# Kernel optimization log

Measured on AMD Instinct MI355X. Metric: run time of the kernel, lower is better.

Reference implementation:

```python
import jax, jax.numpy as jnp
import numpy as np

N = 30000      # node_size / new_node_size
R = 1000       # rel_size
T = 300000     # triple_size (edges)
D = 128        # node_hid == rel_hid
B = 1024       # train pairs
NNZ = 600000   # nnz of ent_adj / rel_adj
DEPTH = 2
GAMMA = 3.0
EPS = 1e-12    # F.normalize eps


def setup_inputs():
    key = jax.random.key(0)
    ks = jax.random.split(key, 12)
    adj = jnp.stack([jax.random.randint(ks[0], (T,), 0, N),
                     jax.random.randint(ks[1], (T,), 0, N)]).astype(jnp.int64)
    # one relation per triple: row ids are 0..T-1, col ids are relation ids
    r_index = jnp.stack([jnp.arange(T),
                         jax.random.randint(ks[2], (T,), 0, R)]).astype(jnp.int64)
    r_val = jnp.ones((T,), jnp.float32)
    ent_adj = jnp.stack([jax.random.randint(ks[3], (NNZ,), 0, N),
                         jax.random.randint(ks[4], (NNZ,), 0, N)]).astype(jnp.int64)
    rel_adj = jnp.stack([jax.random.randint(ks[5], (NNZ,), 0, N),
                         jax.random.randint(ks[6], (NNZ,), 0, R)]).astype(jnp.int64)
    ent_emb = jax.random.normal(ks[7], (N, D), jnp.float32) * 0.05
    rel_emb = jax.random.normal(ks[8], (R, D), jnp.float32) * 0.05
    attn_e = jax.random.normal(ks[9], (DEPTH, D, 1), jnp.float32) * 0.1
    attn_r = jax.random.normal(ks[10], (DEPTH, D, 1), jnp.float32) * 0.1
    train_pairs = jax.random.randint(ks[11], (B, 2), 0, N).astype(jnp.int64)
    return dict(ent_emb=ent_emb, rel_emb=rel_emb, attn_e=attn_e, attn_r=attn_r,
                r_val=r_val, adj=adj, r_index=r_index, ent_adj=ent_adj,
                rel_adj=rel_adj, train_pairs=train_pairs)


def _segment_softmax(vals, seg, num):
    m = jax.ops.segment_max(vals, seg, num_segments=num)
    e = jnp.exp(vals - m[seg])
    s = jax.ops.segment_sum(e, seg, num_segments=num)
    return e / s[seg]


def _avg(adj, emb):
    # sparse softmax of an all-ones matrix over dim=1 == 1/deg per nonzero, then spmm
    row, col = adj[0], adj[1]
    deg = jax.ops.segment_sum(jnp.ones_like(row, emb.dtype), row, num_segments=N)
    return jax.ops.segment_sum(emb[col] / deg[row][:, None], row, num_segments=N)


def _gat(features, rel_emb, adj, r_index, r_val, kernels):
    features = jnp.tanh(features)
    outputs = [features]
    row, col = adj[0], adj[1]
    for l in range(DEPTH):
        # sparse [T,R] @ rel_emb  -> per-triple relation embedding
        tri_rel = jax.ops.segment_sum(r_val[:, None] * rel_emb[r_index[1]],
                                      r_index[0], num_segments=T)          # [T,D]
        tri_rel = tri_rel / jnp.maximum(
            jnp.linalg.norm(tri_rel, axis=1, keepdims=True), EPS)
        neighs = features[col]                                             # [T,D]
        neighs = neighs - 2.0 * jnp.sum(neighs * tri_rel, axis=1,
                                        keepdims=True) * tri_rel
        att = jnp.squeeze(tri_rel @ kernels[l], axis=-1)                   # [T]
        att = _segment_softmax(att, row, N)
        new_features = jax.ops.segment_sum(neighs * att[:, None], row,
                                           num_segments=N)
        features = jnp.tanh(new_features)
        outputs.append(features)
    return jnp.concatenate(outputs, axis=-1)  # [N, (DEPTH+1)*D]


def _align_loss(pairs, emb):
    l, r = pairs[:, 0], pairs[:, 1]
    l_emb, r_emb = emb[l], emb[r]
    pos = jnp.sum(jnp.square(l_emb - r_emb), axis=-1, keepdims=True)       # [B,1]

    def sqdist(A, Bm):
        return (jnp.sum(jnp.square(A), axis=1)[:, None]
                + jnp.sum(jnp.square(Bm), axis=1)[None, :]
                - 2.0 * A @ Bm.T)

    bi = jnp.arange(pairs.shape[0])
    mask = jnp.ones((pairs.shape[0], N), emb.dtype)
    mask = mask.at[bi, l].add(-1.0).at[bi, r].add(-1.0)  # 1 - onehot(l) - onehot(r)

    def norm_lse(loss):
        mu = jax.lax.stop_gradient(jnp.mean(loss, axis=-1, keepdims=True))
        sd = jax.lax.stop_gradient(jnp.std(loss, axis=-1, keepdims=True))
        loss = (loss - mu) / sd
        return jax.nn.logsumexp(20.0 * loss + 8.0, axis=-1)

    l_loss = norm_lse((pos - sqdist(l_emb, emb) + GAMMA) * mask)
    r_loss = norm_lse((pos - sqdist(r_emb, emb) + GAMMA) * mask)
    return jnp.mean(l_loss + r_loss)


def reference(ent_emb, rel_emb, attn_e, attn_r, r_val, adj, r_index,
              ent_adj, rel_adj, train_pairs):
    ent_feature = _avg(ent_adj, ent_emb)   # [N,D]
    rel_feature = _avg(rel_adj, rel_emb)   # [N,D]
    out_rel = _gat(rel_feature, rel_emb, adj, r_index, r_val, attn_r)
    out_ent = _gat(ent_feature, rel_emb, adj, r_index, r_val, attn_e)
    emb = jnp.concatenate([out_ent, out_rel], axis=-1)  # [N, 6*D]
    return _align_loss(train_pairs, emb)
```

## Files before the change

### kernel.cpp

```cpp
#include <hip/hip_runtime.h>
#include <math.h>

#define N_ENT 30000
#define R_REL 1000
#define T_EDGE 300000
#define B_PAIR 1024
#define NNZ_E 600000
#define GAMMAF 3.0f
#define EPSV 1e-12f
#define EMBD 768
#define NPAD 30720
#define NT128 240
#define PTILES 480

typedef _Float16 half8 __attribute__((ext_vector_type(8)));
typedef _Float16 half4v __attribute__((ext_vector_type(4)));
typedef _Float16 half2v __attribute__((ext_vector_type(2)));
typedef float f32x4 __attribute__((ext_vector_type(4)));

__device__ inline void gl_lds16(const _Float16* g, _Float16* l){
  __builtin_amdgcn_global_load_lds(
      (const __attribute__((address_space(1))) unsigned int*)g,
      (__attribute__((address_space(3))) unsigned int*)l, 16, 0, 0);
}

__device__ inline float waveRedSum(float v){
  #pragma unroll
  for(int m=32;m>=1;m>>=1) v += __shfl_xor(v, m, 64);
  return v;
}

__device__ inline float fast_tanh(float x){
  x = fminf(10.f, fmaxf(-10.f, x));
  float e = __expf(2.f*x);
  return (e-1.f)/(e+1.f);
}

__global__ __launch_bounds__(256) void k_count3(const int* __restrict__ rA, int* cA,
                                                const int* __restrict__ rE, int* cE,
                                                const int* __restrict__ rR, int* cR){
  int e = blockIdx.x*256 + threadIdx.x;
  if(e < T_EDGE) atomicAdd(&cA[rA[e]], 1);
  if(e < NNZ_E){ atomicAdd(&cE[rE[e]], 1); atomicAdd(&cR[rR[e]], 1); }
}

__global__ __launch_bounds__(1024) void k_scan3(const int* c0, int* s0, int* u0,
                                                const int* c1, int* s1, int* u1,
                                                const int* c2, int* s2, int* u2){
  const int* cnt = blockIdx.x==0 ? c0 : (blockIdx.x==1 ? c1 : c2);
  int* start     = blockIdx.x==0 ? s0 : (blockIdx.x==1 ? s1 : s2);
  int* cursor    = blockIdx.x==0 ? u0 : (blockIdx.x==1 ? u1 : u2);
  __shared__ int wsum[16];
  __shared__ int carry;
  int tid = threadIdx.x, lane = tid & 63, wid = tid >> 6;
  if(tid==0) carry = 0;
  __syncthreads();
  for(int base=0; base<N_ENT; base+=1024){
    int i = base + tid;
    int v = (i<N_ENT)? cnt[i] : 0;
    int x = v;
    #pragma unroll
    for(int off=1; off<64; off<<=1){ int t=__shfl_up(x,off,64); if(lane>=off) x+=t; }
    if(lane==63) wsum[wid]=x;
    __syncthreads();
    if(wid==0){
      int s = (lane<16)? wsum[lane] : 0;
      #pragma unroll
      for(int off=1; off<16; off<<=1){ int t=__shfl_up(s,off,64); if(lane>=off) s+=t; }
      if(lane<16) wsum[lane]=s;
    }
    __syncthreads();
    int wexcl = (wid==0)? 0 : wsum[wid-1];
    int excl = carry + wexcl + x - v;
    if(i<N_ENT){ start[i]=excl; cursor[i]=excl; }
    int tot = wsum[15];
    __syncthreads();
    if(tid==0) carry += tot;
    __syncthreads();
  }
  if(tid==0) start[N_ENT] = carry;
}

__global__ __launch_bounds__(256) void k_scatter3(
      const int* __restrict__ rA, const int* __restrict__ cAj, const int* __restrict__ rid,
      int* uA, int* scolA, int* sridA,
      const int* __restrict__ rE, const int* __restrict__ cEj, int* uE, int* scolE,
      const int* __restrict__ rR, const int* __restrict__ cRj, int* uR, int* scolR){
  int e = blockIdx.x*256 + threadIdx.x;
  if(e < T_EDGE){
    int p = atomicAdd(&uA[rA[e]], 1);
    scolA[p] = cAj[e];
    sridA[p] = rid[e];
  }
  if(e < NNZ_E){
    int p = atomicAdd(&uE[rE[e]], 1);
    scolE[p] = cEj[e];
    int q = atomicAdd(&uR[rR[e]], 1);
    scolR[q] = cRj[e];
  }
}

__global__ __launch_bounds__(256) void k_avg_tanh(const int* __restrict__ start, const int* __restrict__ scol,
                        const float* __restrict__ src, _Float16* featC, _Float16* Eh, int pairOff, int coloff){
  int r = blockIdx.x*4 + (threadIdx.x>>6);
  int lane = threadIdx.x & 63;
  int s0 = start[r], s1 = start[r+1];
  float ax=0.f, ay=0.f;
  int e = s0;
  for(; e+1<s1; e+=2){
    int c0 = scol[e], c1 = scol[e+1];
    float2 v0 = *(const float2*)(src + (size_t)c0*128 + lane*2);
    float2 v1 = *(const float2*)(src + (size_t)c1*128 + lane*2);
    ax += v0.x + v1.x; ay += v0.y + v1.y;
  }
  if(e<s1){
    int c0 = scol[e];
    float2 v0 = *(const float2*)(src + (size_t)c0*128 + lane*2);
    ax += v0.x; ay += v0.y;
  }
  float inv = (s1>s0) ? 1.0f/(float)(s1-s0) : 0.f;
  float vx = fast_tanh(ax*inv), vy = fast_tanh(ay*inv);
  half2v hv = {(_Float16)vx, (_Float16)vy};
  *(half2v*)(featC + (size_t)r*256 + lane*4 + pairOff) = hv;
  *(half2v*)(Eh + (size_t)r*EMBD + coloff + lane*2) = hv;
}

__global__ __launch_bounds__(256) void k_relnorm(const float* __restrict__ rel, const float* __restrict__ ae,
                          const float* __restrict__ ar, _Float16* relnH, float* expdot){
  int r = (blockIdx.x*256 + threadIdx.x) >> 6;
  int lane = threadIdx.x & 63;
  if (r >= R_REL) return;
  float2 v = *(const float2*)(rel + (size_t)r*128 + lane*2);
  float ss = waveRedSum(v.x*v.x + v.y*v.y);
  float nrm = fmaxf(sqrtf(ss), EPSV);
  float2 u; u.x = v.x/nrm; u.y = v.y/nrm;
  half2v uh = {(_Float16)u.x, (_Float16)u.y};
  *(half2v*)(relnH + (size_t)r*128 + lane*2) = uh;
  const float* ks[4] = {ae, ae+128, ar, ar+128};
  #pragma unroll
  for(int k=0;k<4;k++){
    float2 w = *(const float2*)(ks[k] + lane*2);
    float d = waveRedSum(u.x*w.x + u.y*w.y);
    if(lane==0) expdot[k*R_REL + r] = __expf(d);
  }
}

__global__ __launch_bounds__(256) void k_edge2(const int* __restrict__ start, const int* __restrict__ scol,
      const int* __restrict__ srid, const _Float16* __restrict__ relnH,
      const float* __restrict__ expE, const float* __restrict__ expR,
      const _Float16* __restrict__ featIn, _Float16* featOut, _Float16* Eh, int colEnt, int colRel){
  int r = blockIdx.x*4 + (threadIdx.x>>6);
  int lane = threadIdx.x & 63;
  int s0 = start[r], s1 = start[r+1];
  float aEx=0,aEy=0,aRx=0,aRy=0, swE=0, swR=0;
  int e = s0;
  for(; e+1<s1; e+=2){
    int c0=scol[e], q0=srid[e], c1=scol[e+1], q1=srid[e+1];
    float wE0=expE[q0], wR0=expR[q0], wE1=expE[q1], wR1=expR[q1];
    half2v u0h = *(const half2v*)(relnH + (size_t)q0*128 + lane*2);
    half2v u1h = *(const half2v*)(relnH + (size_t)q1*128 + lane*2);
    half4v h0 = *(const half4v*)(featIn + (size_t)c0*256 + lane*4);
    half4v h1 = *(const half4v*)(featIn + (size_t)c1*256 + lane*4);
    float u0x=(float)u0h[0], u0y=(float)u0h[1], u1x=(float)u1h[0], u1y=(float)u1h[1];
    float e0x=(float)h0[0], e0y=(float)h0[1], r0x=(float)h0[2], r0y=(float)h0[3];
    float e1x=(float)h1[0], e1y=(float)h1[1], r1x=(float)h1[2], r1y=(float)h1[3];
    float d0 = e0x*u0x + e0y*u0y;
    float d1 = r0x*u0x + r0y*u0y;
    float d2 = e1x*u1x + e1y*u1y;
    float d3 = r1x*u1x + r1y*u1y;
    #pragma unroll
    for(int m=32;m>=1;m>>=1){
      d0 += __shfl_xor(d0,m,64); d1 += __shfl_xor(d1,m,64);
      d2 += __shfl_xor(d2,m,64); d3 += __shfl_xor(d3,m,64);
    }
    aEx += wE0*(e0x - 2.f*d0*u0x) + wE1*(e1x - 2.f*d2*u1x);
    aEy += wE0*(e0y - 2.f*d0*u0y) + wE1*(e1y - 2.f*d2*u1y);
    aRx += wR0*(r0x - 2.f*d1*u0x) + wR1*(r1x - 2.f*d3*u1x);
    aRy += wR0*(r0y - 2.f*d1*u0y) + wR1*(r1y - 2.f*d3*u1y);
    swE += wE0+wE1; swR += wR0+wR1;
  }
  if(e<s1){
    int c0=scol[e], q0=srid[e];
    float wE0=expE[q0], wR0=expR[q0];
    half2v u0h = *(const half2v*)(relnH + (size_t)q0*128 + lane*2);
    half4v h0 = *(const half4v*)(featIn + (size_t)c0*256 + lane*4);
    float u0x=(float)u0h[0], u0y=(float)u0h[1];
    float e0x=(float)h0[0], e0y=(float)h0[1], r0x=(float)h0[2], r0y=(float)h0[3];
    float d0 = e0x*u0x + e0y*u0y;
    float d1 = r0x*u0x + r0y*u0y;
    #pragma unroll
    for(int m=32;m>=1;m>>=1){ d0 += __shfl_xor(d0,m,64); d1 += __shfl_xor(d1,m,64); }
    aEx += wE0*(e0x - 2.f*d0*u0x);
    aEy += wE0*(e0y - 2.f*d0*u0y);
    aRx += wR0*(r0x - 2.f*d1*u0x);
    aRy += wR0*(r0y - 2.f*d1*u0y);
    swE += wE0; swR += wR0;
  }
  float iE = (s1>s0) ? 1.f/swE : 0.f;
  float iR = (s1>s0) ? 1.f/swR : 0.f;
  float vEx = fast_tanh(aEx*iE), vEy = fast_tanh(aEy*iE);
  float vRx = fast_tanh(aRx*iR), vRy = fast_tanh(aRy*iR);
  half4v ov = {(_Float16)vEx,(_Float16)vEy,(_Float16)vRx,(_Float16)vRy};
  *(half4v*)(featOut + (size_t)r*256 + lane*4) = ov;
  half2v he = {(_Float16)vEx,(_Float16)vEy};
  half2v hr = {(_Float16)vRx,(_Float16)vRy};
  *(half2v*)(Eh + (size_t)r*EMBD + colEnt + lane*2) = he;
  *(half2v*)(Eh + (size_t)r*EMBD + colRel + lane*2) = hr;
}

__global__ __launch_bounds__(256) void k_gather(const _Float16* __restrict__ Eh, const int* __restrict__ tp,
                         _Float16* Wh, float* cvec){
  int i = blockIdx.x; int tid = threadIdx.x;
  int l = tp[2*i], r = tp[2*i+1];
  float sl=0.f, sr=0.f, sp=0.f;
  for(int c=tid;c<EMBD;c+=256){
    _Float16 lh = Eh[(size_t)l*EMBD+c], rh = Eh[(size_t)r*EMBD+c];
    float le = (float)lh, re = (float)rh;
    Wh[(size_t)i*EMBD+c]=lh; Wh[(size_t)(B_PAIR+i)*EMBD+c]=rh;
    sl += le*le; sr += re*re; float d = le-re; sp += d*d;
  }
  __shared__ float s0[256], s1[256], s2[256];
  s0[tid]=sl; s1[tid]=sr; s2[tid]=sp;
  __syncthreads();
  for(int w=128;w>0;w>>=1){
    if(tid<w){ s0[tid]+=s0[tid+w]; s1[tid]+=s1[tid+w]; s2[tid]+=s2[tid+w]; }
    __syncthreads();
  }
  if(tid==0){
    float pos = s2[0];
    cvec[i]        = pos + GAMMAF - s0[0];
    cvec[B_PAIR+i] = pos + GAMMAF - s1[0];
  }
}

__global__ __launch_bounds__(256) void k_qn(const _Float16* __restrict__ Eh, float* qn){
  int j = (blockIdx.x*256 + threadIdx.x) >> 6;
  int lane = threadIdx.x & 63;
  if(j >= NPAD) return;
  if(j >= N_ENT){ if(lane==0) qn[j] = 1e30f; return; }
  float s=0.f;
  #pragma unroll
  for(int q=0;q<12;q++){ float v = (float)Eh[(size_t)j*EMBD + lane + 64*q]; s += v*v; }
  s = waveRedSum(s);
  if(lane==0) qn[j]=s;
}

__global__ __launch_bounds__(256) void k_embstats(const _Float16* __restrict__ Eh, const float* __restrict__ qn,
                           float* Svec, float* Pvec, float* QQ){
  int tid = threadIdx.x;
  int n0 = blockIdx.x*32;
  int nend = n0+32; if(nend > N_ENT) nend = N_ENT;
  float s[3]={0,0,0}, p[3]={0,0,0};
  float q1=0.f, q2=0.f;
  for(int n=n0;n<nend;n++){
    float qv = qn[n];
    if(tid==0){ q1 += qv; q2 += qv*qv; }
    #pragma unroll
    for(int k=0;k<3;k++){
      float v = (float)Eh[(size_t)n*EMBD + tid + k*256];
      s[k] += v; p[k] += qv*v;
    }
  }
  #pragma unroll
  for(int k=0;k<3;k++){
    unsafeAtomicAdd(&Svec[tid + k*256], s[k]);
    unsafeAtomicAdd(&Pvec[tid + k*256], p[k]);
  }
  if(tid==0){ unsafeAtomicAdd(&QQ[0], q1); unsafeAtomicAdd(&QQ[1], q2); }
}

__global__ __launch_bounds__(256) void k_transp(const _Float16* __restrict__ Eh, _Float16* embT){
  __shared__ __align__(16) _Float16 til[64][72];
  int r0 = blockIdx.x*64, c0 = blockIdx.y*64;
  int t = threadIdx.x;
  int rr = t>>3, c8 = (t&7)*8;
  #pragma unroll
  for(int p=0;p<2;p++){
    int gr = r0 + rr + p*32;
    uint4 v = make_uint4(0u,0u,0u,0u);
    if(gr < N_ENT) v = *(const uint4*)(Eh + (size_t)gr*EMBD + c0 + c8);
    *(uint4*)&til[rr + p*32][c8] = v;
  }
  __syncthreads();
  #pragma unroll
  for(int p=0;p<2;p++){
    int cc = rr + p*32;
    __align__(16) _Float16 tmp[8];
    #pragma unroll
    for(int j=0;j<8;j++) tmp[j] = til[c8 + j][cc];
    *(uint4*)(embT + (size_t)(c0+cc)*NPAD + r0 + c8) = *(uint4*)tmp;
  }
}

__global__ __launch_bounds__(256) void k_syrk(const _Float16* __restrict__ embT, float* G){
  __shared__ __align__(16) _Float16 As[128*64];
  __shared__ __align__(16) _Float16 Bs[128*64];
  int tid = threadIdx.x;
  int w = tid>>6, lane = tid&63;
  int quad = lane>>4, l15 = lane&15;
  int lr = lane>>3, lc = lane&7;
  int wm = (w>>1)*64, wn = (w&1)*64;
  int m0 = blockIdx.y*128, n0 = blockIdx.x*128;
  int kbeg = blockIdx.z*3840;
  int kend = kbeg + 3840; if(kend > NPAD) kend = NPAD;
  f32x4 acc[4][4];
  #pragma unroll
  for(int i=0;i<4;i++)
    #pragma unroll
    for(int j=0;j<4;j++) acc[i][j] = (f32x4){0.f,0.f,0.f,0.f};
  for(int k0=kbeg;k0<kend;k0+=64){
    #pragma unroll
    for(int p=0;p<4;p++){
      int r = p*32 + w*8 + lr;
      int cg = lc ^ (r&7);
      gl_lds16(embT + (size_t)(m0+r)*NPAD + k0 + cg*8, As + (p*32 + w*8)*64);
      gl_lds16(embT + (size_t)(n0+r)*NPAD + k0 + cg*8, Bs + (p*32 + w*8)*64);
    }
    __syncthreads();
    #pragma unroll
    for(int ks=0;ks<2;ks++){
      half8 af[4], bf[4];
      #pragma unroll
      for(int i=0;i<4;i++){
        int ml = wm + i*16 + l15;
        af[i] = *(half8*)(As + ml*64 + (((ks<<2)|quad) ^ (ml&7))*8);
      }
      #pragma unroll
      for(int j=0;j<4;j++){
        int nl = wn + j*16 + l15;
        bf[j] = *(half8*)(Bs + nl*64 + (((ks<<2)|quad) ^ (nl&7))*8);
      }
      #pragma unroll
      for(int i=0;i<4;i++)
        #pragma unroll
        for(int j=0;j<4;j++)
          acc[i][j] = __builtin_amdgcn_mfma_f32_16x16x32_f16(af[i], bf[j], acc[i][j], 0,0,0);
    }
    __syncthreads();
  }
  #pragma unroll
  for(int i=0;i<4;i++){
    #pragma unroll
    for(int r=0;r<4;r++){
      int m = m0 + wm + i*16 + quad*4 + r;
      #pragma unroll
      for(int j=0;j<4;j++){
        int n = n0 + wn + j*16 + l15;
        unsafeAtomicAdd(&G[(size_t)m*EMBD + n], acc[i][j][r]);
      }
    }
  }
}

__global__ __launch_bounds__(256) void k_cvtG(const float* __restrict__ G, _Float16* Gh){
  int i = blockIdx.x*256 + threadIdx.x;
  if(i < EMBD*EMBD) Gh[i] = (_Float16)G[i];
}

__device__ inline void mfma_k768(const _Float16* __restrict__ Asrc, const _Float16* __restrict__ Bsrc,
                                 int m0, int n0, int l15, int quad, f32x4 acc[4][4]){
  const _Float16* aB[4]; const _Float16* bB[4];
  #pragma unroll
  for(int i=0;i<4;i++){
    aB[i] = Asrc + (size_t)(m0+i*16+l15)*EMBD + quad*8;
    bB[i] = Bsrc + (size_t)(n0+i*16+l15)*EMBD + quad*8;
  }
  half8 af[2][4], bf[2][4];
  #pragma unroll
  for(int i=0;i<4;i++){ af[0][i] = *(const half8*)(aB[i]); bf[0][i] = *(const half8*)(bB[i]); }
  #pragma unroll
  for(int ks=0; ks<24; ks++){
    int cur = ks&1, nxt = cur^1;
    if(ks<23){
      int ko = (ks+1)*32;
      #pragma unroll
      for(int i=0;i<4;i++){ af[nxt][i] = *(const half8*)(aB[i]+ko); bf[nxt][i] = *(const half8*)(bB[i]+ko); }
    }
    #pragma unroll
    for(int i=0;i<4;i++)
      #pragma unroll
      for(int j=0;j<4;j++)
        acc[i][j] = __builtin_amdgcn_mfma_f32_16x16x32_f16(af[cur][i], bf[cur][j], acc[i][j], 0,0,0);
  }
}

__global__ __launch_bounds__(256) void k_gemmTh(const _Float16* __restrict__ Wh, const _Float16* __restrict__ Gh,
                                                float* Tm){
  int tid = threadIdx.x, w = tid>>6, lane = tid&63;
  int quad = lane>>4, l15 = lane&15;
  int n0 = blockIdx.x*64;
  #pragma unroll
  for(int half=0; half<2; half++){
    int mt = blockIdx.y*8 + half*4 + w;
    int m0 = mt*64;
    f32x4 acc[4][4];
    #pragma unroll
    for(int i=0;i<4;i++)
      #pragma unroll
      for(int j=0;j<4;j++) acc[i][j] = (f32x4){0.f,0.f,0.f,0.f};
    mfma_k768(Wh, Gh, m0, n0, l15, quad, acc);
    #pragma unroll
    for(int i=0;i<4;i++)
      #pragma unroll
      for(int r=0;r<4;r++){
        int mg = m0 + i*16 + quad*4 + r;
        #pragma unroll
        for(int j=0;j<4;j++)
          Tm[(size_t)mg*EMBD + n0 + j*16 + l15] = acc[i][j][r];
      }
  }
}

__global__ __launch_bounds__(256) void k_rowstats(const _Float16* __restrict__ Wh, const float* __restrict__ Tm,
      const _Float16* __restrict__ Eh, const float* __restrict__ qn, const float* __restrict__ cvec,
      const int* __restrict__ tp, const float* __restrict__ Svec, const float* __restrict__ Pvec,
      const float* __restrict__ QQ, float* alpha, float* betav){
  int row = blockIdx.x*4 + (threadIdx.x>>6);
  int lane = threadIdx.x & 63;
  if(row >= 2*B_PAIR) return;
  int pi = row & (B_PAIR-1);
  int lp = tp[2*pi], rp = tp[2*pi+1];
  float d1=0,d2=0,d3=0,dl=0,dr=0;
  #pragma unroll
  for(int k=0;k<12;k++){
    int d = lane + 64*k;
    float a = (float)Wh[(size_t)row*EMBD + d];
    d1 += a*Svec[d];
    d2 += a*Pvec[d];
    d3 += a*Tm[(size_t)row*EMBD + d];
    dl += a*(float)Eh[(size_t)lp*EMBD + d];
    dr += a*(float)Eh[(size_t)rp*EMBD + d];
  }
  d1=waveRedSum(d1); d2=waveRedSum(d2); d3=waveRedSum(d3);
  dl=waveRedSum(dl); dr=waveRedSum(dr);
  if(lane==0){
    double c = (double)cvec[row], Q = (double)QQ[0], Q2 = (double)QQ[1], Nn = (double)N_ENT;
    double su  = Nn*c - Q + 2.0*(double)d1;
    double su2 = Nn*c*c - 2.0*c*Q + Q2 + 4.0*(c*(double)d1 - (double)d2) + 4.0*(double)d3;
    double ul = c - (double)qn[lp] + 2.0*(double)dl;
    double ur = c - (double)qn[rp] + 2.0*(double)dr;
    su -= ul + ur;
    if(lp != rp) su2 -= ul*ul + ur*ur;
    double mu = su/Nn;
    double var = su2/Nn - mu*mu;
    double sd = sqrt(fmax(var, 0.0));
    double al = 20.0/sd;
    alpha[row] = (float)al;
    betav[row] = (float)(8.0 - al*mu);
  }
}

__device__ inline void lseMerge(float& mx, float& sm, float om, float os){
  if(om > mx){ sm = sm*expf(mx-om) + os; mx = om; }
  else if(om != -INFINITY){ sm += os*expf(om-mx); }
}

__global__ __launch_bounds__(256) void k_gemmB(const _Float16* __restrict__ Wh, const _Float16* __restrict__ Eh,
    const float* __restrict__ cvec, const float* __restrict__ qn, const int* __restrict__ tp,
    const float* __restrict__ alpha, const float* __restrict__ betav, float* pm, float* ps){
  __shared__ __align__(16) _Float16 As[128*64];
  __shared__ __align__(16) _Float16 Bs[128*64];
  int id = blockIdx.x;
  int ntile = (id & 7) + ((id >> 7) << 3);
  int m0 = ((id >> 3) & 15) * 128;
  int n0 = ntile * 128;
  int tid = threadIdx.x;
  int w = tid>>6, lane = tid&63;
  int quad = lane>>4, l15 = lane&15;
  int lr = lane>>3, lc = lane&7;
  int wm = (w&1)*64, wn = (w>>1)*64;
  f32x4 acc[4][4];
  #pragma unroll
  for(int i=0;i<4;i++)
    #pragma unroll
    for(int j=0;j<4;j++) acc[i][j] = (f32x4){0.f,0.f,0.f,0.f};
  for(int k0=0;k0<EMBD;k0+=64){
    #pragma unroll
    for(int p=0;p<4;p++){
      int r = p*32 + w*8 + lr;
      int cg = lc ^ (r&7);
      gl_lds16(Wh + (size_t)(m0+r)*EMBD + k0 + cg*8, As + (p*32 + w*8)*64);
      gl_lds16(Eh + (size_t)(n0+r)*EMBD + k0 + cg*8, Bs + (p*32 + w*8)*64);
    }
    __syncthreads();
    #pragma unroll
    for(int ks=0;ks<2;ks++){
      half8 af[4], bf[4];
      #pragma unroll
      for(int i=0;i<4;i++){
        int ml = wm + i*16 + l15;
        af[i] = *(half8*)(As + ml*64 + (((ks<<2)|quad) ^ (ml&7))*8);
      }
      #pragma unroll
      for(int j=0;j<4;j++){
        int nl = wn + j*16 + l15;
        bf[j] = *(half8*)(Bs + nl*64 + (((ks<<2)|quad) ^ (nl&7))*8);
      }
      #pragma unroll
      for(int i=0;i<4;i++)
        #pragma unroll
        for(int j=0;j<4;j++)
          acc[i][j] = __builtin_amdgcn_mfma_f32_16x16x32_f16(af[i], bf[j], acc[i][j], 0,0,0);
    }
    __syncthreads();
  }
  float qv[4]; int jv[4];
  #pragma unroll
  for(int j=0;j<4;j++){ jv[j] = n0 + wn + j*16 + l15; qv[j] = qn[jv[j]]; }
  int ptile = ntile*2 + (w>>1);
  #pragma unroll
  for(int i=0;i<4;i++){
    int mbase = m0 + wm + i*16 + quad*4;
    #pragma unroll
    for(int r=0;r<4;r++){
      int mg = mbase + r;
      int pi = mg & (B_PAIR-1);
      int lp = tp[2*pi], rp = tp[2*pi+1];
      float cv = cvec[mg], al = alpha[mg], be = betav[mg];
      float mx = -INFINITY, sm = 0.f;
      #pragma unroll
      for(int j=0;j<4;j++){
        float u = fmaf(2.f, acc[i][j][r], cv - qv[j]);
        float z = fmaf(al, u, be);
        if(jv[j]==lp || jv[j]==rp) z = (lp==rp) ? fmaf(-al, u, be) : be;
        if(z > mx){ sm = sm*__expf(mx - z) + 1.f; mx = z; }
        else sm += __expf(z - mx);
      }
      #pragma unroll
      for(int m=8;m>=1;m>>=1){
        float om = __shfl_xor(mx, m, 64), os = __shfl_xor(sm, m, 64);
        lseMerge(mx, sm, om, os);
      }
      if(l15==0){ pm[(size_t)mg*PTILES + ptile] = mx; ps[(size_t)mg*PTILES + ptile] = sm; }
    }
  }
}

__global__ __launch_bounds__(256) void k_lse(const float* __restrict__ pm, const float* __restrict__ ps, float* lse){
  __shared__ float shm[256], shs[256];
  int row = blockIdx.x, tid = threadIdx.x;
  float mx = -INFINITY, sm = 0.f;
  for(int t=tid;t<PTILES;t+=256) lseMerge(mx, sm, pm[(size_t)row*PTILES+t], ps[(size_t)row*PTILES+t]);
  shm[tid]=mx; shs[tid]=sm;
  __syncthreads();
  for(int w=128;w>0;w>>=1){
    if(tid<w){
      float m2=shm[tid], s2=shs[tid];
      lseMerge(m2, s2, shm[tid+w], shs[tid+w]);
      shm[tid]=m2; shs[tid]=s2;
    }
    __syncthreads();
  }
  if(tid==0) lse[row] = shm[0] + logf(shs[0]);
}

__global__ __launch_bounds__(256) void k_final(const float* __restrict__ lse, float* out){
  __shared__ double sh[256];
  int tid = threadIdx.x;
  double s = 0.0;
  for(int i=tid;i<B_PAIR;i+=256) s += (double)lse[i] + (double)lse[B_PAIR+i];
  sh[tid]=s; __syncthreads();
  for(int w=128;w>0;w>>=1){ if(tid<w) sh[tid]+=sh[tid+w]; __syncthreads(); }
  if(tid==0) out[0] = (float)(sh[0] / (double)B_PAIR);
}

extern "C" void kernel_launch(void* const* d_in, const int* in_sizes, int n_in,
                              void* d_out, int out_size, void* d_ws, size_t ws_size,
                              hipStream_t stream) {
  const float* ent_emb = (const float*)d_in[0];
  const float* rel_emb = (const float*)d_in[1];
  const float* attn_e  = (const float*)d_in[2];
  const float* attn_r  = (const float*)d_in[3];
  const int* adj     = (const int*)d_in[5];
  const int* r_index = (const int*)d_in[6];
  const int* ent_adj = (const int*)d_in[7];
  const int* rel_adj = (const int*)d_in[8];
  const int* tp      = (const int*)d_in[9];
  float* out = (float*)d_out;

  const int* adj_row = adj;
  const int* adj_col = adj + T_EDGE;
  const int* rid1    = r_index + T_EDGE;

  char* base = (char*)d_ws;
  size_t off = 0;
  auto A = [&](size_t b)->void*{ void* p = base + off; off = (off + b + 255) & ~(size_t)255; return p; };
  int*   cntA  = (int*)  A((size_t)N_ENT*4);
  int*   cntE  = (int*)  A((size_t)N_ENT*4);
  int*   cntR  = (int*)  A((size_t)N_ENT*4);
  float* G     = (float*)A((size_t)EMBD*EMBD*4);
  float* Svec  = (float*)A(EMBD*4);
  float* Pvec  = (float*)A(EMBD*4);
  float* QQ    = (float*)A(2*4);
  size_t zero_end = off;
  int* startA = (int*)A((size_t)(N_ENT+1)*4);
  int* startE = (int*)A((size_t)(N_ENT+1)*4);
  int* startR = (int*)A((size_t)(N_ENT+1)*4);
  int* curA   = (int*)A((size_t)N_ENT*4);
  int* curE   = (int*)A((size_t)N_ENT*4);
  int* curR   = (int*)A((size_t)N_ENT*4);
  int* scolA  = (int*)A((size_t)T_EDGE*4);
  int* sridA  = (int*)A((size_t)T_EDGE*4);
  int* scolE  = (int*)A((size_t)NNZ_E*4);
  int* scolR  = (int*)A((size_t)NNZ_E*4);
  _Float16* Eh = (_Float16*)A((size_t)NPAD*EMBD*2);
  char* X = (char*)A((size_t)EMBD*NPAD*2);
  _Float16* featC0 = (_Float16*)X;
  _Float16* featC1 = (_Float16*)(X + 16u*1024u*1024u);
  _Float16* embT   = (_Float16*)X;
  float*    pm     = (float*)X;
  float*    ps     = (float*)(X + 8u*1024u*1024u);
  _Float16* relnH  = (_Float16*)A((size_t)R_REL*128*2);
  float* expdot  = (float*)A(4*R_REL*4);
  _Float16* Wh   = (_Float16*)A((size_t)2*B_PAIR*EMBD*2);
  _Float16* Gh   = (_Float16*)A((size_t)EMBD*EMBD*2);
  float* Tm      = (float*)A((size_t)2*B_PAIR*EMBD*4);
  float* cvec    = (float*)A(2*B_PAIR*4);
  float* qn      = (float*)A((size_t)NPAD*4);
  float* alpha   = (float*)A(2*B_PAIR*4);
  float* betav   = (float*)A(2*B_PAIR*4);
  float* lse     = (float*)A(2*B_PAIR*4);
  (void)ws_size; (void)in_sizes; (void)n_in; (void)out_size;

  hipMemsetAsync(d_ws, 0, zero_end, stream);
  hipMemsetAsync(Eh + (size_t)N_ENT*EMBD, 0, (size_t)(NPAD-N_ENT)*EMBD*2, stream);

  k_count3<<<(NNZ_E+255)/256, 256, 0, stream>>>(adj_row, cntA, ent_adj, cntE, rel_adj, cntR);
  k_scan3<<<3, 1024, 0, stream>>>(cntA, startA, curA, cntE, startE, curE, cntR, startR, curR);
  k_scatter3<<<(NNZ_E+255)/256, 256, 0, stream>>>(adj_row, adj_col, rid1, curA, scolA, sridA,
                                                  ent_adj, ent_adj+NNZ_E, curE, scolE,
                                                  rel_adj, rel_adj+NNZ_E, curR, scolR);

  k_relnorm<<<R_REL/4, 256, 0, stream>>>(rel_emb, attn_e, attn_r, relnH, expdot);

  k_avg_tanh<<<N_ENT/4, 256, 0, stream>>>(startE, scolE, ent_emb, featC0, Eh, 0, 0);
  k_avg_tanh<<<N_ENT/4, 256, 0, stream>>>(startR, scolR, rel_emb, featC0, Eh, 2, 384);
  k_edge2<<<N_ENT/4, 256, 0, stream>>>(startA, scolA, sridA, relnH, expdot + 0*R_REL, expdot + 2*R_REL,
                                       featC0, featC1, Eh, 128, 512);
  k_edge2<<<N_ENT/4, 256, 0, stream>>>(startA, scolA, sridA, relnH, expdot + 1*R_REL, expdot + 3*R_REL,
                                       featC1, featC0, Eh, 256, 640);

  k_gather<<<B_PAIR, 256, 0, stream>>>(Eh, tp, Wh, cvec);
  k_qn<<<NPAD/4, 256, 0, stream>>>(Eh, qn);
  k_embstats<<<(N_ENT+31)/32, 256, 0, stream>>>(Eh, qn, Svec, Pvec, QQ);
  dim3 gtr(NPAD/64, 12);
  k_transp<<<gtr, 256, 0, stream>>>(Eh, embT);
  dim3 gsy(6, 6, 8);
  k_syrk<<<gsy, 256, 0, stream>>>(embT, G);
  k_cvtG<<<(EMBD*EMBD+255)/256, 256, 0, stream>>>(G, Gh);
  dim3 gT(EMBD/64, 4);
  k_gemmTh<<<gT, 256, 0, stream>>>(Wh, Gh, Tm);
  k_rowstats<<<2*B_PAIR/4, 256, 0, stream>>>(Wh, Tm, Eh, qn, cvec, tp, Svec, Pvec, QQ, alpha, betav);
  k_gemmB<<<NT128*16, 256, 0, stream>>>(Wh, Eh, cvec, qn, tp, alpha, betav, pm, ps);
  k_lse<<<2*B_PAIR, 256, 0, stream>>>(pm, ps, lse);
  k_final<<<1, 256, 0, stream>>>(lse, out);
}
```

Baseline: 949.4 us.

## Enlarge gemmB M tile to 256, gather fp16 embeddings, fuse avg launches

The main GEMM now uses a 256x128 tile, so each wave holds 8x4 MFMA accumulators and the Eh tiles are reused across twice as many query rows, halving the block count. Entity and relation embeddings are first converted to fp16 in a new kernel, so the neighbor-averaging gathers move half the bytes. The two averaging launches are merged into one 2D grid. The trade-offs are higher register pressure and LDS use in gemmB (launch bounds now ask for 2 blocks), an extra conversion pass, and a small precision loss in the averaged features.

```diff
diff --git a/kernel.cpp b/kernel.cpp
--- a/kernel.cpp
+++ b/kernel.cpp
@@ -100,8 +100,24 @@
   }
 }
 
-__global__ __launch_bounds__(256) void k_avg_tanh(const int* __restrict__ start, const int* __restrict__ scol,
-                        const float* __restrict__ src, _Float16* featC, _Float16* Eh, int pairOff, int coloff){
+__global__ __launch_bounds__(256) void k_cvtemb(const float* __restrict__ ent, const float* __restrict__ rel,
+                                                _Float16* ehE, _Float16* ehR){
+  int i = blockIdx.x*256 + threadIdx.x;
+  if(i < N_ENT*128) ehE[i] = (_Float16)ent[i];
+  if(i < R_REL*128) ehR[i] = (_Float16)rel[i];
+}
+
+__global__ __launch_bounds__(256) void k_avg2(const int* __restrict__ startE, const int* __restrict__ scolE,
+                        const _Float16* __restrict__ srcE,
+                        const int* __restrict__ startR, const int* __restrict__ scolR,
+                        const _Float16* __restrict__ srcR,
+                        _Float16* featC, _Float16* Eh){
+  int which = blockIdx.y;
+  const int* start = which? startR : startE;
+  const int* scol  = which? scolR : scolE;
+  const _Float16* src = which? srcR : srcE;
+  int pairOff = which? 2 : 0;
+  int coloff  = which? 384 : 0;
   int r = blockIdx.x*4 + (threadIdx.x>>6);
   int lane = threadIdx.x & 63;
   int s0 = start[r], s1 = start[r+1];
@@ -109,14 +125,14 @@
   int e = s0;
   for(; e+1<s1; e+=2){
     int c0 = scol[e], c1 = scol[e+1];
-    float2 v0 = *(const float2*)(src + (size_t)c0*128 + lane*2);
-    float2 v1 = *(const float2*)(src + (size_t)c1*128 + lane*2);
-    ax += v0.x + v1.x; ay += v0.y + v1.y;
+    half2v v0 = *(const half2v*)(src + (size_t)c0*128 + lane*2);
+    half2v v1 = *(const half2v*)(src + (size_t)c1*128 + lane*2);
+    ax += (float)v0[0] + (float)v1[0]; ay += (float)v0[1] + (float)v1[1];
   }
   if(e<s1){
     int c0 = scol[e];
-    float2 v0 = *(const float2*)(src + (size_t)c0*128 + lane*2);
-    ax += v0.x; ay += v0.y;
+    half2v v0 = *(const half2v*)(src + (size_t)c0*128 + lane*2);
+    ax += (float)v0[0]; ay += (float)v0[1];
   }
   float inv = (s1>s0) ? 1.0f/(float)(s1-s0) : 0.f;
   float vx = fast_tanh(ax*inv), vy = fast_tanh(ay*inv);
@@ -455,39 +471,44 @@
   else if(om != -INFINITY){ sm += os*expf(om-mx); }
 }
 
-__global__ __launch_bounds__(256) void k_gemmB(const _Float16* __restrict__ Wh, const _Float16* __restrict__ Eh,
+__global__ __launch_bounds__(256,2) void k_gemmB(const _Float16* __restrict__ Wh, const _Float16* __restrict__ Eh,
     const float* __restrict__ cvec, const float* __restrict__ qn, const int* __restrict__ tp,
     const float* __restrict__ alpha, const float* __restrict__ betav, float* pm, float* ps){
-  __shared__ __align__(16) _Float16 As[128*64];
+  __shared__ __align__(16) _Float16 As[256*64];
   __shared__ __align__(16) _Float16 Bs[128*64];
   int id = blockIdx.x;
-  int ntile = (id & 7) + ((id >> 7) << 3);
-  int m0 = ((id >> 3) & 15) * 128;
+  int ntile = (id & 7) + ((id >> 6) << 3);
+  int m0 = ((id >> 3) & 7) * 256;
   int n0 = ntile * 128;
   int tid = threadIdx.x;
   int w = tid>>6, lane = tid&63;
   int quad = lane>>4, l15 = lane&15;
   int lr = lane>>3, lc = lane&7;
-  int wm = (w&1)*64, wn = (w>>1)*64;
-  f32x4 acc[4][4];
-  #pragma unroll
-  for(int i=0;i<4;i++)
+  int wm = (w&1)*128, wn = (w>>1)*64;
+  f32x4 acc[8][4];
+  #pragma unroll
+  for(int i=0;i<8;i++)
     #pragma unroll
     for(int j=0;j<4;j++) acc[i][j] = (f32x4){0.f,0.f,0.f,0.f};
   for(int k0=0;k0<EMBD;k0+=64){
+    #pragma unroll
+    for(int p=0;p<8;p++){
+      int r = p*32 + w*8 + lr;
+      int cg = lc ^ (r&7);
+      gl_lds16(Wh + (size_t)(m0+r)*EMBD + k0 + cg*8, As + (p*32 + w*8)*64);
+    }
     #pragma unroll
     for(int p=0;p<4;p++){
       int r = p*32 + w*8 + lr;
       int cg = lc ^ (r&7);
-      gl_lds16(Wh + (size_t)(m0+r)*EMBD + k0 + cg*8, As + (p*32 + w*8)*64);
       gl_lds16(Eh + (size_t)(n0+r)*EMBD + k0 + cg*8, Bs + (p*32 + w*8)*64);
     }
     __syncthreads();
     #pragma unroll
     for(int ks=0;ks<2;ks++){
-      half8 af[4], bf[4];
-      #pragma unroll
-      for(int i=0;i<4;i++){
+      half8 af[8], bf[4];
+      #pragma unroll
+      for(int i=0;i<8;i++){
         int ml = wm + i*16 + l15;
         af[i] = *(half8*)(As + ml*64 + (((ks<<2)|quad) ^ (ml&7))*8);
       }
@@ -497,7 +518,7 @@
         bf[j] = *(half8*)(Bs + nl*64 + (((ks<<2)|quad) ^ (nl&7))*8);
       }
       #pragma unroll
-      for(int i=0;i<4;i++)
+      for(int i=0;i<8;i++)
         #pragma unroll
         for(int j=0;j<4;j++)
           acc[i][j] = __builtin_amdgcn_mfma_f32_16x16x32_f16(af[i], bf[j], acc[i][j], 0,0,0);
@@ -509,7 +530,7 @@
   for(int j=0;j<4;j++){ jv[j] = n0 + wn + j*16 + l15; qv[j] = qn[jv[j]]; }
   int ptile = ntile*2 + (w>>1);
   #pragma unroll
-  for(int i=0;i<4;i++){
+  for(int i=0;i<8;i++){
     int mbase = m0 + wm + i*16 + quad*4;
     #pragma unroll
     for(int r=0;r<4;r++){
@@ -611,6 +632,8 @@
   float*    pm     = (float*)X;
   float*    ps     = (float*)(X + 8u*1024u*1024u);
   _Float16* relnH  = (_Float16*)A((size_t)R_REL*128*2);
+  _Float16* ehE   = (_Float16*)A((size_t)N_ENT*128*2);
+  _Float16* ehR   = (_Float16*)A((size_t)R_REL*128*2);
   float* expdot  = (float*)A(4*R_REL*4);
   _Float16* Wh   = (_Float16*)A((size_t)2*B_PAIR*EMBD*2);
   _Float16* Gh   = (_Float16*)A((size_t)EMBD*EMBD*2);
@@ -631,10 +654,11 @@
                                                   ent_adj, ent_adj+NNZ_E, curE, scolE,
                                                   rel_adj, rel_adj+NNZ_E, curR, scolR);
 
+  k_cvtemb<<<(N_ENT*128+255)/256, 256, 0, stream>>>(ent_emb, rel_emb, ehE, ehR);
   k_relnorm<<<R_REL/4, 256, 0, stream>>>(rel_emb, attn_e, attn_r, relnH, expdot);
 
-  k_avg_tanh<<<N_ENT/4, 256, 0, stream>>>(startE, scolE, ent_emb, featC0, Eh, 0, 0);
-  k_avg_tanh<<<N_ENT/4, 256, 0, stream>>>(startR, scolR, rel_emb, featC0, Eh, 2, 384);
+  dim3 gavg(N_ENT/4, 2);
+  k_avg2<<<gavg, 256, 0, stream>>>(startE, scolE, ehE, startR, scolR, ehR, featC0, Eh);
   k_edge2<<<N_ENT/4, 256, 0, stream>>>(startA, scolA, sridA, relnH, expdot + 0*R_REL, expdot + 2*R_REL,
                                        featC0, featC1, Eh, 128, 512);
   k_edge2<<<N_ENT/4, 256, 0, stream>>>(startA, scolA, sridA, relnH, expdot + 1*R_REL, expdot + 3*R_REL,
@@ -651,7 +675,7 @@
   dim3 gT(EMBD/64, 4);
   k_gemmTh<<<gT, 256, 0, stream>>>(Wh, Gh, Tm);
   k_rowstats<<<2*B_PAIR/4, 256, 0, stream>>>(Wh, Tm, Eh, qn, cvec, tp, Svec, Pvec, QQ, alpha, betav);
-  k_gemmB<<<NT128*16, 256, 0, stream>>>(Wh, Eh, cvec, qn, tp, alpha, betav, pm, ps);
+  k_gemmB<<<NT128*8, 256, 0, stream>>>(Wh, Eh, cvec, qn, tp, alpha, betav, pm, ps);
   k_lse<<<2*B_PAIR, 256, 0, stream>>>(pm, ps, lse);
   k_final<<<1, 256, 0, stream>>>(lse, out);
 }
```

Result: faster. 915.2 us (-3.6%).
